# Optimization experiments

Measured on AMD Instinct MI355X. Metric: run time of the kernel, lower is better.

Reference implementation:

```python
import jax, jax.numpy as jnp
import numpy as np

N = 4096
IN_DIM = 256
OUT_DIM = 256
E = 131072


def setup_inputs() -> dict:
    key = jax.random.key(0)
    ks = jax.random.split(key, 8)
    x = jax.random.normal(ks[0], (N, IN_DIM), dtype=jnp.float32)
    edge_index = jax.random.randint(ks[1], (2, E), 0, N, dtype=jnp.int64)
    lap = jax.random.normal(ks[2], (N, N), dtype=jnp.float32)
    d_inv = jax.random.normal(ks[3], (N, N), dtype=jnp.float32)
    # parameters
    W_high = jax.random.normal(ks[4], (IN_DIM, OUT_DIM), dtype=jnp.float32) / np.sqrt(IN_DIM)
    W_conv = jax.random.normal(ks[5], (IN_DIM, OUT_DIM), dtype=jnp.float32) / np.sqrt(IN_DIM)
    b_conv = jnp.zeros((OUT_DIM,), dtype=jnp.float32)
    aL = jax.random.uniform(ks[6], (1,), dtype=jnp.float32)
    aH = jax.random.uniform(ks[7], (1,), dtype=jnp.float32)
    return {"x": x, "edge_index": edge_index, "lap": lap, "d_inv": d_inv,
            "W_high": W_high, "W_conv": W_conv, "b_conv": b_conv,
            "aL": aL, "aH": aH}


def _gcn_conv(x, edge_index, W, b, num_nodes):
    # PyG GCNConv: add self-loops, symmetric normalization, aggregate at target.
    src, dst = edge_index[0], edge_index[1]
    loop = jnp.arange(num_nodes, dtype=edge_index.dtype)
    src_f = jnp.concatenate([src, loop])
    dst_f = jnp.concatenate([dst, loop])
    deg = jax.ops.segment_sum(jnp.ones_like(dst_f, dtype=x.dtype), dst_f,
                              num_segments=num_nodes)
    deg_inv_sqrt = jnp.where(deg > 0, jax.lax.rsqrt(jnp.maximum(deg, 1e-12)), 0.0)
    norm = deg_inv_sqrt[src_f] * deg_inv_sqrt[dst_f]  # [E+N]
    xw = x @ W                                        # [N, out]
    msgs = xw[src_f] * norm[:, None]                  # [E+N, out]
    out = jax.ops.segment_sum(msgs, dst_f, num_segments=num_nodes)
    return out + b


def reference(x, edge_index, lap, d_inv, W_high, W_conv, b_conv, aL, aH):
    # high-pass branch: Lhp = d_inv @ lap @ d_inv; Hh = Lhp @ relu(x @ W_high)
    Lhp = (d_inv @ lap) @ d_inv
    Hh = Lhp @ jax.nn.relu(x @ W_high)
    # low-pass branch: GCNConv
    Hl = _gcn_conv(x, edge_index, W_conv, b_conv, x.shape[0])
    return aL * Hl + aH * Hh
```

## Files before the change

### kernel.cpp

```cpp
#include <hip/hip_runtime.h>

#define NN 4096
#define DD 256
#define EE 131072

typedef __attribute__((ext_vector_type(8))) short s16x8;
typedef __attribute__((ext_vector_type(4))) float f32x4;

__device__ __forceinline__ unsigned short f2bf(float f) {
  unsigned u = __builtin_bit_cast(unsigned, f);
  u += 0x7FFFu + ((u >> 16) & 1u);
  return (unsigned short)(u >> 16);
}

__device__ __forceinline__ ushort4 cvt4(f32x4 v) {
  ushort4 r;
  r.x = f2bf(v[0]); r.y = f2bf(v[1]); r.z = f2bf(v[2]); r.w = f2bf(v[3]);
  return r;
}

__device__ __forceinline__ unsigned cvt2_rhu(float a, float b) {
  unsigned ua = __builtin_bit_cast(unsigned, a) + 0x8000u;
  unsigned ub = __builtin_bit_cast(unsigned, b) + 0x8000u;
  return __builtin_amdgcn_perm(ub, ua, 0x07060302u);
}

__device__ __forceinline__ uint4 pack8(f32x4 a, f32x4 b) {
  uint4 r;
  r.x = cvt2_rhu(a[0], a[1]); r.y = cvt2_rhu(a[2], a[3]);
  r.z = cvt2_rhu(b[0], b[1]); r.w = cvt2_rhu(b[2], b[3]);
  return r;
}


__global__ void k_prep(const int* __restrict__ ei, int* __restrict__ deg,
                       const float* __restrict__ Wh, const float* __restrict__ Wc,
                       unsigned short* __restrict__ WFh, unsigned short* __restrict__ WFc) {
  int t = blockIdx.x * 256 + threadIdx.x;
  if (t < EE) {
    atomicAdd(&deg[ei[EE + t]], 1);
  } else {
    int idx = t - EE;
    int which = idx >> 16;
    int r = idx & 65535;
    int n = r & 255, k = r >> 8;
    const float* W = which ? Wc : Wh;
    unsigned short* WF = which ? WFc : WFh;
    long fidx = ((long)((n >> 4) * 8 + (k >> 5))) * 512 +
                (((k >> 3) & 3) * 16 + (n & 15)) * 8 + (k & 7);
    WF[fidx] = f2bf(W[k * 256 + n]);
  }
}

__global__ void k_scan(const int* __restrict__ deg, int* __restrict__ row_start,
                       float* __restrict__ dis) {
  __shared__ int part[1024];
  int t = threadIdx.x;
  int d0 = deg[4 * t + 0], d1 = deg[4 * t + 1], d2 = deg[4 * t + 2], d3 = deg[4 * t + 3];
  int s = d0 + d1 + d2 + d3;
  part[t] = s;
  __syncthreads();
  for (int off = 1; off < 1024; off <<= 1) {
    int add = (t >= off) ? part[t - off] : 0;
    __syncthreads();
    part[t] += add;
    __syncthreads();
  }
  int base = part[t] - s;
  row_start[4 * t + 0] = base;
  row_start[4 * t + 1] = base + d0;
  row_start[4 * t + 2] = base + d0 + d1;
  row_start[4 * t + 3] = base + d0 + d1 + d2;
  if (t == 1023) row_start[4096] = part[t];
  dis[4 * t + 0] = rsqrtf((float)d0 + 1.0f);
  dis[4 * t + 1] = rsqrtf((float)d1 + 1.0f);
  dis[4 * t + 2] = rsqrtf((float)d2 + 1.0f);
  dis[4 * t + 3] = rsqrtf((float)d3 + 1.0f);
}

__global__ void k_scatter(const int* __restrict__ ei, const int* __restrict__ row_start,
                          int* __restrict__ cursor, int* __restrict__ csr) {
  int e = blockIdx.x * 256 + threadIdx.x;
  if (e < EE) {
    int s = ei[e];
    int d = ei[EE + e];
    int p = atomicAdd(&cursor[d], 1);
    csr[row_start[d] + p] = s;
  }
}

__global__ __launch_bounds__(512) void k_xw(const float* __restrict__ x,
                                            const unsigned short* __restrict__ WFh,
                                            const unsigned short* __restrict__ WFc,
                                            unsigned short* __restrict__ RF,
                                            float* __restrict__ XWs,
                                            const float* __restrict__ dis) {
  __shared__ alignas(16) unsigned short Abuf[16][264];
  const int tid = threadIdx.x;
  const int w = tid >> 6, lane = tid & 63;
  const int quad = lane >> 4, l16 = lane & 15, quad8 = quad * 8;
  const int m0 = blockIdx.x * 16;

  {
    int srow = tid >> 5, scolf = (tid & 31) * 8;
    const float* ap = x + (long)(m0 + srow) * DD + scolf;
    f32x4 a0 = *(const f32x4*)ap;
    f32x4 a1 = *(const f32x4*)(ap + 4);
    *(uint4*)&Abuf[srow][scolf] = pack8(a0, a1);
  }
  __syncthreads();

  const bool hi = (w < 4);
  const int wo = hi ? w : (w - 4);
  const unsigned short* WF = hi ? WFh : WFc;
  const unsigned short* bp = WF + lane * 8;

  f32x4 acc[4] = {{0,0,0,0},{0,0,0,0},{0,0,0,0},{0,0,0,0}};
#pragma unroll
  for (int q = 0; q < 8; ++q) {
    s16x8 af = *(const s16x8*)&Abuf[l16][q * 32 + quad8];
#pragma unroll
    for (int s = 0; s < 4; ++s) {
      s16x8 bf = *(const s16x8*)(bp + ((long)((4 * wo + s) * 8 + q)) * 512);
      acc[s] = __builtin_amdgcn_mfma_f32_16x16x32_bf16(af, bf, acc[s], 0, 0, 0);
    }
  }

  if (hi) {
    const int kc = m0 >> 5;
    const int qp = ((m0 >> 4) & 1) * 2 + (quad >> 1);
    const int j0 = (quad & 1) * 4;
#pragma unroll
    for (int s = 0; s < 4; ++s) {
      int t = 4 * wo + s;
      f32x4 v = acc[s];
      f32x4 z;
      z[0] = v[0] > 0.f ? v[0] : 0.f;
      z[1] = v[1] > 0.f ? v[1] : 0.f;
      z[2] = v[2] > 0.f ? v[2] : 0.f;
      z[3] = v[3] > 0.f ? v[3] : 0.f;
      long idx = ((long)(t * 128 + kc)) * 512 + (qp * 16 + l16) * 8 + j0;
      *(ushort4*)(RF + idx) = cvt4(z);
    }
  } else {
    float dm[4];
#pragma unroll
    for (int r = 0; r < 4; ++r) dm[r] = dis[m0 + quad * 4 + r];
#pragma unroll
    for (int s = 0; s < 4; ++s) {
      int col = 64 * wo + 16 * s + l16;
#pragma unroll
      for (int r = 0; r < 4; ++r)
        XWs[(long)(m0 + quad * 4 + r) * DD + col] = dm[r] * acc[s][r];
    }
  }
}

__global__ void k_agg(const float* __restrict__ XWs, const int* __restrict__ row_start,
                      const int* __restrict__ csr, const float* __restrict__ dis,
                      float* __restrict__ Hl) {
  const int i = blockIdx.x;
  const int t = threadIdx.x;
  const int b0 = row_start[i], b1 = row_start[i + 1];
  float acc = XWs[(long)i * DD + t];
  int j = b0;
  for (; j + 4 <= b1; j += 4) {
    int s0 = csr[j], s1 = csr[j + 1], s2 = csr[j + 2], s3 = csr[j + 3];
    float v0 = XWs[(long)s0 * DD + t];
    float v1 = XWs[(long)s1 * DD + t];
    float v2 = XWs[(long)s2 * DD + t];
    float v3 = XWs[(long)s3 * DD + t];
    acc += (v0 + v1) + (v2 + v3);
  }
  for (; j < b1; ++j) acc += XWs[(long)csr[j] * DD + t];
  Hl[(long)i * DD + t] = dis[i] * acc;
}

template <int EPI>
__global__ __launch_bounds__(512) void k_mm2(const float* __restrict__ A,
                                             const unsigned short* __restrict__ BF,
                                             unsigned short* __restrict__ CF,
                                             float* __restrict__ outF,
                                             const float* __restrict__ Hl,
                                             const float* __restrict__ bconv,
                                             const float* __restrict__ aLp,
                                             const float* __restrict__ aHp) {
  __shared__ alignas(16) unsigned short Abuf[2][32][264];
  const int tid = threadIdx.x;
  const int w = tid >> 6, lane = tid & 63;
  const int quad = lane >> 4, l16 = lane & 15, quad8 = quad * 8;
  const int tile = blockIdx.x & 127, half = blockIdx.x >> 7;
  const int m0 = tile * 32;
  const int tglob = half * 8 + w;

  const int arow = tid >> 4;
  const int acolf = (tid & 15) * 16;
  const float* aptr = A + (long)(m0 + arow) * NN + acolf;

  {
    f32x4 c0 = *(const f32x4*)(aptr + 0);
    f32x4 c1 = *(const f32x4*)(aptr + 4);
    f32x4 c2 = *(const f32x4*)(aptr + 8);
    f32x4 c3 = *(const f32x4*)(aptr + 12);
    *(uint4*)&Abuf[0][arow][acolf] = pack8(c0, c1);
    *(uint4*)&Abuf[0][arow][acolf + 8] = pack8(c2, c3);
  }
  f32x4 anext[4];
#pragma unroll
  for (int i = 0; i < 4; ++i) anext[i] = *(const f32x4*)(aptr + 256 + 4 * i);
  __syncthreads();

  f32x4 acc[2] = {{0,0,0,0},{0,0,0,0}};
  const unsigned short* bbase = BF + ((long)tglob * 128) * 512 + lane * 8;

  for (int s = 0; s < 16; ++s) {
    const int cur = s & 1;
    f32x4 afut[4];
    if (s + 2 < 16) {
#pragma unroll
      for (int i = 0; i < 4; ++i)
        afut[i] = *(const f32x4*)(aptr + (s + 2) * 256 + 4 * i);
    } else {
#pragma unroll
      for (int i = 0; i < 4; ++i) afut[i] = anext[i];
    }

    const unsigned short* bs = bbase + ((long)s * 8) * 512;
#pragma unroll
    for (int c8 = 0; c8 < 8; ++c8) {
      s16x8 bf = *(const s16x8*)(bs + c8 * 512);
      s16x8 a0 = *(const s16x8*)&Abuf[cur][l16][c8 * 32 + quad8];
      s16x8 a1 = *(const s16x8*)&Abuf[cur][16 + l16][c8 * 32 + quad8];
      acc[0] = __builtin_amdgcn_mfma_f32_16x16x32_bf16(a0, bf, acc[0], 0, 0, 0);
      acc[1] = __builtin_amdgcn_mfma_f32_16x16x32_bf16(a1, bf, acc[1], 0, 0, 0);
    }

    if (s + 1 < 16) {
      *(uint4*)&Abuf[1 - cur][arow][acolf] = pack8(anext[0], anext[1]);
      *(uint4*)&Abuf[1 - cur][arow][acolf + 8] = pack8(anext[2], anext[3]);
    }
    __syncthreads();
#pragma unroll
    for (int i = 0; i < 4; ++i) anext[i] = afut[i];
  }

  if constexpr (EPI == 0) {
    const int kc = m0 >> 5;
#pragma unroll
    for (int mu = 0; mu < 2; ++mu) {
      int qp = mu * 2 + (quad >> 1);
      int j0 = (quad & 1) * 4;
      long idx = ((long)(tglob * 128 + kc)) * 512 + (qp * 16 + l16) * 8 + j0;
      *(ushort4*)(CF + idx) = cvt4(acc[mu]);
    }
  } else {
    __shared__ float obuf[32][132];
#pragma unroll
    for (int mu = 0; mu < 2; ++mu)
#pragma unroll
      for (int r = 0; r < 4; ++r)
        obuf[mu * 16 + quad * 4 + r][w * 16 + l16] = acc[mu][r];
    __syncthreads();
    const float aLv = aLp[0], aHv = aHp[0];
    const int orow = tid >> 4;
    const int ocol = (tid & 15) * 8;
    const int gcol = half * 128 + ocol;
#pragma unroll
    for (int j = 0; j < 2; ++j) {
      f32x4 cc = *(const f32x4*)&obuf[orow][ocol + 4 * j];
      f32x4 h = *(const f32x4*)(Hl + (long)(m0 + orow) * DD + gcol + 4 * j);
      f32x4 bc = *(const f32x4*)(bconv + gcol + 4 * j);
      f32x4 res;
      res[0] = aHv * cc[0] + aLv * (h[0] + bc[0]);
      res[1] = aHv * cc[1] + aLv * (h[1] + bc[1]);
      res[2] = aHv * cc[2] + aLv * (h[2] + bc[2]);
      res[3] = aHv * cc[3] + aLv * (h[3] + bc[3]);
      *(f32x4*)(outF + (long)(m0 + orow) * DD + gcol + 4 * j) = res;
    }
  }
}

extern "C" void kernel_launch(void* const* d_in, const int* in_sizes, int n_in,
                              void* d_out, int out_size, void* d_ws, size_t ws_size,
                              hipStream_t stream) {
  const float* x     = (const float*)d_in[0];
  const int*   ei    = (const int*)d_in[1];
  const float* lap   = (const float*)d_in[2];
  const float* dinv  = (const float*)d_in[3];
  const float* Wh    = (const float*)d_in[4];
  const float* Wc    = (const float*)d_in[5];
  const float* bconv = (const float*)d_in[6];
  const float* aL    = (const float*)d_in[7];
  const float* aH    = (const float*)d_in[8];
  float* out = (float*)d_out;
  char* ws = (char*)d_ws;

  int* deg        = (int*)(ws);
  int* cursor     = (int*)(ws + (16 << 10));
  int* row_start  = (int*)(ws + (32 << 10));
  int* csr        = (int*)(ws + (64 << 10));
  float* dis      = (float*)(ws + (576 << 10));
  unsigned short* WFh = (unsigned short*)(ws + (1l << 20));
  unsigned short* WFc = (unsigned short*)(ws + (1l << 20) + (128 << 10));
  unsigned short* RF  = (unsigned short*)(ws + (2l << 20));
  unsigned short* T1F = (unsigned short*)(ws + (4l << 20));
  unsigned short* T2F = (unsigned short*)(ws + (6l << 20));
  float* XWs = (float*)(ws + (8l << 20));
  float* Hl  = (float*)(ws + (12l << 20));

  hipMemsetAsync(ws, 0, 32 << 10, stream);

  k_prep<<<1024, 256, 0, stream>>>(ei, deg, Wh, Wc, WFh, WFc);
  k_scan<<<1, 1024, 0, stream>>>(deg, row_start, dis);
  k_scatter<<<512, 256, 0, stream>>>(ei, row_start, cursor, csr);
  k_xw<<<256, 512, 0, stream>>>(x, WFh, WFc, RF, XWs, dis);
  k_agg<<<4096, 256, 0, stream>>>(XWs, row_start, csr, dis, Hl);

  k_mm2<0><<<256, 512, 0, stream>>>(dinv, RF, T1F, nullptr, nullptr, nullptr, nullptr, nullptr);
  k_mm2<0><<<256, 512, 0, stream>>>(lap, T1F, T2F, nullptr, nullptr, nullptr, nullptr, nullptr);
  k_mm2<3><<<256, 512, 0, stream>>>(dinv, T2F, nullptr, out, Hl, bconv, aL, aH);
}
```

Before: 273.9 us.

## Densify GCN aggregation into normalized adjacency GEMM and split-K all GEMMs

Replaces the CSR build and gather-based aggregation with a dense normalized adjacency matrix M, built by atomic scatter in fragment layout, so the low-pass branch becomes a GEMM. All four 4096x4096x256 products now use a split-K GEMM with 128x256 register tiles, followed by separate reduction kernels. The first dinv GEMM also emits dinv as bf16 fragments so the final GEMM can skip re-converting it. This costs a 64MB memset, a dense GEMM over a mostly-zero matrix, and large partial-sum traffic in exchange for higher MFMA utilization and no irregular gathers.

```diff
diff --git a/kernel.cpp b/kernel.cpp
--- a/kernel.cpp
+++ b/kernel.cpp
@@ -25,11 +25,11 @@
   return __builtin_amdgcn_perm(ub, ua, 0x07060302u);
 }
 
-__device__ __forceinline__ uint4 pack8(f32x4 a, f32x4 b) {
-  uint4 r;
-  r.x = cvt2_rhu(a[0], a[1]); r.y = cvt2_rhu(a[2], a[3]);
-  r.z = cvt2_rhu(b[0], b[1]); r.w = cvt2_rhu(b[2], b[3]);
-  return r;
+__device__ __forceinline__ s16x8 frag_from(f32x4 a, f32x4 b) {
+  uint4 u;
+  u.x = cvt2_rhu(a[0], a[1]); u.y = cvt2_rhu(a[2], a[3]);
+  u.z = cvt2_rhu(b[0], b[1]); u.w = cvt2_rhu(b[2], b[3]);
+  return __builtin_bit_cast(s16x8, u);
 }
 
 
@@ -47,45 +47,31 @@
     const float* W = which ? Wc : Wh;
     unsigned short* WF = which ? WFc : WFh;
     long fidx = ((long)((n >> 4) * 8 + (k >> 5))) * 512 +
-                (((k >> 3) & 3) * 16 + (n & 15)) * 8 + (k & 7);
+                (((k >> 3) & 3) * 128 + (n & 15) * 8 + (k & 7));
     WF[fidx] = f2bf(W[k * 256 + n]);
   }
 }
 
-__global__ void k_scan(const int* __restrict__ deg, int* __restrict__ row_start,
-                       float* __restrict__ dis) {
-  __shared__ int part[1024];
-  int t = threadIdx.x;
-  int d0 = deg[4 * t + 0], d1 = deg[4 * t + 1], d2 = deg[4 * t + 2], d3 = deg[4 * t + 3];
-  int s = d0 + d1 + d2 + d3;
-  part[t] = s;
-  __syncthreads();
-  for (int off = 1; off < 1024; off <<= 1) {
-    int add = (t >= off) ? part[t - off] : 0;
-    __syncthreads();
-    part[t] += add;
-    __syncthreads();
-  }
-  int base = part[t] - s;
-  row_start[4 * t + 0] = base;
-  row_start[4 * t + 1] = base + d0;
-  row_start[4 * t + 2] = base + d0 + d1;
-  row_start[4 * t + 3] = base + d0 + d1 + d2;
-  if (t == 1023) row_start[4096] = part[t];
-  dis[4 * t + 0] = rsqrtf((float)d0 + 1.0f);
-  dis[4 * t + 1] = rsqrtf((float)d1 + 1.0f);
-  dis[4 * t + 2] = rsqrtf((float)d2 + 1.0f);
-  dis[4 * t + 3] = rsqrtf((float)d3 + 1.0f);
-}
-
-__global__ void k_scatter(const int* __restrict__ ei, const int* __restrict__ row_start,
-                          int* __restrict__ cursor, int* __restrict__ csr) {
+__global__ void k_dis(const int* __restrict__ deg, float* __restrict__ dis,
+                      float* __restrict__ M) {
+  int i = blockIdx.x * 256 + threadIdx.x;
+  float d = rsqrtf((float)deg[i] + 1.0f);
+  dis[i] = d;
+  long idx = ((long)((i >> 4) * 128 + (i >> 5))) * 512 +
+             (((i >> 3) & 3) * 128 + (i & 15) * 8 + (i & 7));
+  atomicAdd(&M[idx], d * d);
+}
+
+__global__ void k_scatterM(const int* __restrict__ ei, const float* __restrict__ dis,
+                           float* __restrict__ M) {
   int e = blockIdx.x * 256 + threadIdx.x;
   if (e < EE) {
     int s = ei[e];
     int d = ei[EE + e];
-    int p = atomicAdd(&cursor[d], 1);
-    csr[row_start[d] + p] = s;
+    float v = dis[d] * dis[s];
+    long idx = ((long)((d >> 4) * 128 + (s >> 5))) * 512 +
+               (((s >> 3) & 3) * 128 + (d & 15) * 8 + (s & 7));
+    atomicAdd(&M[idx], v);
   }
 }
 
@@ -93,8 +79,7 @@
                                             const unsigned short* __restrict__ WFh,
                                             const unsigned short* __restrict__ WFc,
                                             unsigned short* __restrict__ RF,
-                                            float* __restrict__ XWs,
-                                            const float* __restrict__ dis) {
+                                            unsigned short* __restrict__ XWcF) {
   __shared__ alignas(16) unsigned short Abuf[16][264];
   const int tid = threadIdx.x;
   const int w = tid >> 6, lane = tid & 63;
@@ -106,13 +91,17 @@
     const float* ap = x + (long)(m0 + srow) * DD + scolf;
     f32x4 a0 = *(const f32x4*)ap;
     f32x4 a1 = *(const f32x4*)(ap + 4);
-    *(uint4*)&Abuf[srow][scolf] = pack8(a0, a1);
+    uint4 u;
+    u.x = cvt2_rhu(a0[0], a0[1]); u.y = cvt2_rhu(a0[2], a0[3]);
+    u.z = cvt2_rhu(a1[0], a1[1]); u.w = cvt2_rhu(a1[2], a1[3]);
+    *(uint4*)&Abuf[srow][scolf] = u;
   }
   __syncthreads();
 
   const bool hi = (w < 4);
   const int wo = hi ? w : (w - 4);
   const unsigned short* WF = hi ? WFh : WFc;
+  unsigned short* OUT = hi ? RF : XWcF;
   const unsigned short* bp = WF + lane * 8;
 
   f32x4 acc[4] = {{0,0,0,0},{0,0,0,0},{0,0,0,0},{0,0,0,0}};
@@ -126,158 +115,181 @@
     }
   }
 
-  if (hi) {
-    const int kc = m0 >> 5;
-    const int qp = ((m0 >> 4) & 1) * 2 + (quad >> 1);
-    const int j0 = (quad & 1) * 4;
-#pragma unroll
-    for (int s = 0; s < 4; ++s) {
-      int t = 4 * wo + s;
-      f32x4 v = acc[s];
-      f32x4 z;
-      z[0] = v[0] > 0.f ? v[0] : 0.f;
-      z[1] = v[1] > 0.f ? v[1] : 0.f;
-      z[2] = v[2] > 0.f ? v[2] : 0.f;
-      z[3] = v[3] > 0.f ? v[3] : 0.f;
-      long idx = ((long)(t * 128 + kc)) * 512 + (qp * 16 + l16) * 8 + j0;
-      *(ushort4*)(RF + idx) = cvt4(z);
-    }
-  } else {
-    float dm[4];
-#pragma unroll
-    for (int r = 0; r < 4; ++r) dm[r] = dis[m0 + quad * 4 + r];
-#pragma unroll
-    for (int s = 0; s < 4; ++s) {
-      int col = 64 * wo + 16 * s + l16;
-#pragma unroll
-      for (int r = 0; r < 4; ++r)
-        XWs[(long)(m0 + quad * 4 + r) * DD + col] = dm[r] * acc[s][r];
-    }
-  }
-}
-
-__global__ void k_agg(const float* __restrict__ XWs, const int* __restrict__ row_start,
-                      const int* __restrict__ csr, const float* __restrict__ dis,
-                      float* __restrict__ Hl) {
-  const int i = blockIdx.x;
-  const int t = threadIdx.x;
-  const int b0 = row_start[i], b1 = row_start[i + 1];
-  float acc = XWs[(long)i * DD + t];
-  int j = b0;
-  for (; j + 4 <= b1; j += 4) {
-    int s0 = csr[j], s1 = csr[j + 1], s2 = csr[j + 2], s3 = csr[j + 3];
-    float v0 = XWs[(long)s0 * DD + t];
-    float v1 = XWs[(long)s1 * DD + t];
-    float v2 = XWs[(long)s2 * DD + t];
-    float v3 = XWs[(long)s3 * DD + t];
-    acc += (v0 + v1) + (v2 + v3);
-  }
-  for (; j < b1; ++j) acc += XWs[(long)csr[j] * DD + t];
-  Hl[(long)i * DD + t] = dis[i] * acc;
-}
-
-template <int EPI>
-__global__ __launch_bounds__(512) void k_mm2(const float* __restrict__ A,
-                                             const unsigned short* __restrict__ BF,
-                                             unsigned short* __restrict__ CF,
-                                             float* __restrict__ outF,
-                                             const float* __restrict__ Hl,
-                                             const float* __restrict__ bconv,
-                                             const float* __restrict__ aLp,
-                                             const float* __restrict__ aHp) {
-  __shared__ alignas(16) unsigned short Abuf[2][32][264];
+  const int kc = m0 >> 5;
+  const int qp = ((m0 >> 4) & 1) * 2 + (quad >> 1);
+  const int j0 = (quad & 1) * 4;
+#pragma unroll
+  for (int s = 0; s < 4; ++s) {
+    int t = 4 * wo + s;
+    f32x4 v = acc[s];
+    if (hi) {
+      v[0] = v[0] > 0.f ? v[0] : 0.f;
+      v[1] = v[1] > 0.f ? v[1] : 0.f;
+      v[2] = v[2] > 0.f ? v[2] : 0.f;
+      v[3] = v[3] > 0.f ? v[3] : 0.f;
+    }
+    long idx = ((long)(t * 128 + kc)) * 512 + (qp * 16 + l16) * 8 + j0;
+    *(ushort4*)(OUT + idx) = cvt4(v);
+  }
+}
+
+template <int AMODE, int EMIT>
+__global__ __launch_bounds__(512) void k_gemm(const float* __restrict__ Afp,
+                                              const unsigned short* __restrict__ AFin,
+                                              const unsigned short* __restrict__ BF,
+                                              float* __restrict__ P,
+                                              unsigned short* __restrict__ AFout) {
   const int tid = threadIdx.x;
   const int w = tid >> 6, lane = tid & 63;
-  const int quad = lane >> 4, l16 = lane & 15, quad8 = quad * 8;
-  const int tile = blockIdx.x & 127, half = blockIdx.x >> 7;
-  const int m0 = tile * 32;
-  const int tglob = half * 8 + w;
-
-  const int arow = tid >> 4;
-  const int acolf = (tid & 15) * 16;
-  const float* aptr = A + (long)(m0 + arow) * NN + acolf;
-
-  {
-    f32x4 c0 = *(const f32x4*)(aptr + 0);
-    f32x4 c1 = *(const f32x4*)(aptr + 4);
-    f32x4 c2 = *(const f32x4*)(aptr + 8);
-    f32x4 c3 = *(const f32x4*)(aptr + 12);
-    *(uint4*)&Abuf[0][arow][acolf] = pack8(c0, c1);
-    *(uint4*)&Abuf[0][arow][acolf + 8] = pack8(c2, c3);
-  }
-  f32x4 anext[4];
-#pragma unroll
-  for (int i = 0; i < 4; ++i) anext[i] = *(const f32x4*)(aptr + 256 + 4 * i);
-  __syncthreads();
-
-  f32x4 acc[2] = {{0,0,0,0},{0,0,0,0}};
-  const unsigned short* bbase = BF + ((long)tglob * 128) * 512 + lane * 8;
-
-  for (int s = 0; s < 16; ++s) {
-    const int cur = s & 1;
-    f32x4 afut[4];
-    if (s + 2 < 16) {
-#pragma unroll
-      for (int i = 0; i < 4; ++i)
-        afut[i] = *(const f32x4*)(aptr + (s + 2) * 256 + 4 * i);
+  const int quad = lane >> 4, l16 = lane & 15;
+  const int mgrp = blockIdx.x & 31, ks = blockIdx.x >> 5;
+  const int m0 = mgrp * 128;
+  const int mh = w & 1, nq = w >> 1;
+  const int kc0 = ks * 16;
+
+  const long mtile0 = (long)(mgrp * 8 + mh * 4);
+  const unsigned short* bptr = BF + (((long)(nq * 4) * 128 + kc0) << 9) + lane * 8;
+  const unsigned short* aptrF = AFin + ((mtile0 * 128 + kc0) << 9) + lane * 8;
+  const float* aptrR = Afp + (long)(m0 + mh * 64 + l16) * NN + kc0 * 32 + quad * 8;
+  const float* aptr2 = Afp + ((mtile0 * 128 + kc0) << 9) + lane * 8;
+  unsigned short* aout = AFout + ((mtile0 * 128 + kc0) << 9) + lane * 8;
+
+  f32x4 acc[4][4];
+#pragma unroll
+  for (int mi = 0; mi < 4; ++mi)
+#pragma unroll
+    for (int ti = 0; ti < 4; ++ti) acc[mi][ti] = (f32x4){0, 0, 0, 0};
+
+  s16x8 bfr[2][4];
+  s16x8 afr[2][4];
+  f32x4 arw[2][8];
+
+#define LOADB(buf, kcv)                                                         \
+  _Pragma("unroll") for (int ti = 0; ti < 4; ++ti)                              \
+      bfr[buf][ti] = *(const s16x8*)(bptr + (((long)(ti * 128 + (kcv))) << 9));
+
+#define LOADA(buf, kcv)                                                         \
+  if (AMODE == 0) {                                                             \
+    _Pragma("unroll") for (int mi = 0; mi < 4; ++mi)                            \
+        afr[buf][mi] = *(const s16x8*)(aptrF + (((long)(mi * 128 + (kcv))) << 9)); \
+  } else if (AMODE == 1) {                                                      \
+    _Pragma("unroll") for (int mi = 0; mi < 4; ++mi) {                          \
+      arw[buf][2 * mi] = *(const f32x4*)(aptrR + (long)mi * 16 * NN + (kcv) * 32); \
+      arw[buf][2 * mi + 1] = *(const f32x4*)(aptrR + (long)mi * 16 * NN + (kcv) * 32 + 4); \
+    }                                                                           \
+  } else {                                                                      \
+    _Pragma("unroll") for (int mi = 0; mi < 4; ++mi) {                          \
+      arw[buf][2 * mi] = *(const f32x4*)(aptr2 + (((long)(mi * 128 + (kcv))) << 9)); \
+      arw[buf][2 * mi + 1] = *(const f32x4*)(aptr2 + (((long)(mi * 128 + (kcv))) << 9) + 4); \
+    }                                                                           \
+  }
+
+  LOADB(0, 0)
+  LOADA(0, 0)
+
+#pragma unroll
+  for (int kc = 0; kc < 16; ++kc) {
+    const int cur = kc & 1, nxt = cur ^ 1;
+    if (kc < 15) {
+      LOADB(nxt, kc + 1)
+      LOADA(nxt, kc + 1)
+    }
+    s16x8 A4[4];
+    if (AMODE == 0) {
+#pragma unroll
+      for (int mi = 0; mi < 4; ++mi) A4[mi] = afr[cur][mi];
     } else {
 #pragma unroll
-      for (int i = 0; i < 4; ++i) afut[i] = anext[i];
-    }
-
-    const unsigned short* bs = bbase + ((long)s * 8) * 512;
-#pragma unroll
-    for (int c8 = 0; c8 < 8; ++c8) {
-      s16x8 bf = *(const s16x8*)(bs + c8 * 512);
-      s16x8 a0 = *(const s16x8*)&Abuf[cur][l16][c8 * 32 + quad8];
-      s16x8 a1 = *(const s16x8*)&Abuf[cur][16 + l16][c8 * 32 + quad8];
-      acc[0] = __builtin_amdgcn_mfma_f32_16x16x32_bf16(a0, bf, acc[0], 0, 0, 0);
-      acc[1] = __builtin_amdgcn_mfma_f32_16x16x32_bf16(a1, bf, acc[1], 0, 0, 0);
-    }
-
-    if (s + 1 < 16) {
-      *(uint4*)&Abuf[1 - cur][arow][acolf] = pack8(anext[0], anext[1]);
-      *(uint4*)&Abuf[1 - cur][arow][acolf + 8] = pack8(anext[2], anext[3]);
-    }
-    __syncthreads();
-#pragma unroll
-    for (int i = 0; i < 4; ++i) anext[i] = afut[i];
-  }
-
-  if constexpr (EPI == 0) {
-    const int kc = m0 >> 5;
-#pragma unroll
-    for (int mu = 0; mu < 2; ++mu) {
-      int qp = mu * 2 + (quad >> 1);
-      int j0 = (quad & 1) * 4;
-      long idx = ((long)(tglob * 128 + kc)) * 512 + (qp * 16 + l16) * 8 + j0;
-      *(ushort4*)(CF + idx) = cvt4(acc[mu]);
-    }
-  } else {
-    __shared__ float obuf[32][132];
-#pragma unroll
-    for (int mu = 0; mu < 2; ++mu)
+      for (int mi = 0; mi < 4; ++mi)
+        A4[mi] = frag_from(arw[cur][2 * mi], arw[cur][2 * mi + 1]);
+    }
+    if (EMIT) {
+      if (nq == 0) {
+#pragma unroll
+        for (int mi = 0; mi < 4; ++mi)
+          *(s16x8*)(aout + (((long)(mi * 128 + kc)) << 9)) = A4[mi];
+      }
+    }
+#pragma unroll
+    for (int ti = 0; ti < 4; ++ti)
+#pragma unroll
+      for (int mi = 0; mi < 4; ++mi)
+        acc[mi][ti] = __builtin_amdgcn_mfma_f32_16x16x32_bf16(A4[mi], bfr[cur][ti], acc[mi][ti], 0, 0, 0);
+  }
+#undef LOADA
+#undef LOADB
+
+  float* pb = P + (long)ks * NN * DD;
+#pragma unroll
+  for (int mi = 0; mi < 4; ++mi) {
+    const int row = m0 + mh * 64 + mi * 16 + quad * 4;
+#pragma unroll
+    for (int ti = 0; ti < 4; ++ti) {
+      const int col = nq * 64 + ti * 16 + l16;
 #pragma unroll
       for (int r = 0; r < 4; ++r)
-        obuf[mu * 16 + quad * 4 + r][w * 16 + l16] = acc[mu][r];
-    __syncthreads();
-    const float aLv = aLp[0], aHv = aHp[0];
-    const int orow = tid >> 4;
-    const int ocol = (tid & 15) * 8;
-    const int gcol = half * 128 + ocol;
-#pragma unroll
-    for (int j = 0; j < 2; ++j) {
-      f32x4 cc = *(const f32x4*)&obuf[orow][ocol + 4 * j];
-      f32x4 h = *(const f32x4*)(Hl + (long)(m0 + orow) * DD + gcol + 4 * j);
-      f32x4 bc = *(const f32x4*)(bconv + gcol + 4 * j);
-      f32x4 res;
-      res[0] = aHv * cc[0] + aLv * (h[0] + bc[0]);
-      res[1] = aHv * cc[1] + aLv * (h[1] + bc[1]);
-      res[2] = aHv * cc[2] + aLv * (h[2] + bc[2]);
-      res[3] = aHv * cc[3] + aLv * (h[3] + bc[3]);
-      *(f32x4*)(outF + (long)(m0 + orow) * DD + gcol + 4 * j) = res;
-    }
-  }
+        pb[(long)(row + r) * DD + col] = acc[mi][ti][r];
+    }
+  }
+}
+
+__global__ void k_redF(const float* __restrict__ P, unsigned short* __restrict__ TF) {
+  const int tid = threadIdx.x;
+  const int w = tid >> 6, lane = tid & 63;
+  const int quad = lane >> 4, l16 = lane & 15;
+#pragma unroll
+  for (int c = 0; c < 2; ++c) {
+    int cid = blockIdx.x * 8 + w * 2 + c;
+    int ntile = cid >> 7, kchunk = cid & 127;
+    int n = ntile * 16 + l16;
+    int kbase = kchunk * 32 + quad * 8;
+    float v[8];
+#pragma unroll
+    for (int j = 0; j < 8; ++j) v[j] = 0.f;
+#pragma unroll
+    for (int s = 0; s < 8; ++s) {
+      const float* p = P + (long)s * NN * DD;
+#pragma unroll
+      for (int j = 0; j < 8; ++j) v[j] += p[(long)(kbase + j) * DD + n];
+    }
+    ushort4 o0, o1;
+    o0.x = f2bf(v[0]); o0.y = f2bf(v[1]); o0.z = f2bf(v[2]); o0.w = f2bf(v[3]);
+    o1.x = f2bf(v[4]); o1.y = f2bf(v[5]); o1.z = f2bf(v[6]); o1.w = f2bf(v[7]);
+    *(ushort4*)(TF + (long)cid * 512 + lane * 8) = o0;
+    *(ushort4*)(TF + (long)cid * 512 + lane * 8 + 4) = o1;
+  }
+}
+
+__global__ void k_redHl(const float* __restrict__ P, float* __restrict__ Hl) {
+  long off = ((long)blockIdx.x * 256 + threadIdx.x) * 4;
+  f32x4 v = {0, 0, 0, 0};
+#pragma unroll
+  for (int s = 0; s < 8; ++s) {
+    f32x4 p = *(const f32x4*)(P + (long)s * NN * DD + off);
+    v[0] += p[0]; v[1] += p[1]; v[2] += p[2]; v[3] += p[3];
+  }
+  *(f32x4*)(Hl + off) = v;
+}
+
+__global__ void k_final(const float* __restrict__ P, const float* __restrict__ Hl,
+                        const float* __restrict__ bconv, const float* __restrict__ aLp,
+                        const float* __restrict__ aHp, float* __restrict__ out) {
+  long off = ((long)blockIdx.x * 256 + threadIdx.x) * 4;
+  f32x4 v = {0, 0, 0, 0};
+#pragma unroll
+  for (int s = 0; s < 8; ++s) {
+    f32x4 p = *(const f32x4*)(P + (long)s * NN * DD + off);
+    v[0] += p[0]; v[1] += p[1]; v[2] += p[2]; v[3] += p[3];
+  }
+  const float aLv = aLp[0], aHv = aHp[0];
+  f32x4 h = *(const f32x4*)(Hl + off);
+  f32x4 b = *(const f32x4*)(bconv + (int)(off & 255));
+  f32x4 res;
+  res[0] = aHv * v[0] + aLv * (h[0] + b[0]);
+  res[1] = aHv * v[1] + aLv * (h[1] + b[1]);
+  res[2] = aHv * v[2] + aLv * (h[2] + b[2]);
+  res[3] = aHv * v[3] + aLv * (h[3] + b[3]);
+  *(f32x4*)(out + off) = res;
 }
 
 extern "C" void kernel_launch(void* const* d_in, const int* in_sizes, int n_in,
@@ -294,29 +306,39 @@
   const float* aH    = (const float*)d_in[8];
   float* out = (float*)d_out;
   char* ws = (char*)d_ws;
-
-  int* deg        = (int*)(ws);
-  int* cursor     = (int*)(ws + (16 << 10));
-  int* row_start  = (int*)(ws + (32 << 10));
-  int* csr        = (int*)(ws + (64 << 10));
-  float* dis      = (float*)(ws + (576 << 10));
-  unsigned short* WFh = (unsigned short*)(ws + (1l << 20));
-  unsigned short* WFc = (unsigned short*)(ws + (1l << 20) + (128 << 10));
-  unsigned short* RF  = (unsigned short*)(ws + (2l << 20));
-  unsigned short* T1F = (unsigned short*)(ws + (4l << 20));
-  unsigned short* T2F = (unsigned short*)(ws + (6l << 20));
-  float* XWs = (float*)(ws + (8l << 20));
-  float* Hl  = (float*)(ws + (12l << 20));
-
-  hipMemsetAsync(ws, 0, 32 << 10, stream);
+  const long MB = 1l << 20;
+
+  float* M              = (float*)(ws);
+  unsigned short* dinvF = (unsigned short*)(ws);
+  float* P              = (float*)(ws + 64 * MB);
+  unsigned short* WFh   = (unsigned short*)(ws + 96 * MB);
+  unsigned short* WFc   = (unsigned short*)(ws + 96 * MB + 128 * 1024);
+  unsigned short* RF    = (unsigned short*)(ws + 97 * MB);
+  unsigned short* XWcF  = (unsigned short*)(ws + 99 * MB);
+  unsigned short* T1F   = (unsigned short*)(ws + 101 * MB);
+  unsigned short* T2F   = (unsigned short*)(ws + 103 * MB);
+  float* Hl             = (float*)(ws + 105 * MB);
+  int* deg              = (int*)(ws + 109 * MB);
+  float* dis            = (float*)(ws + 109 * MB + 16 * 1024);
+
+  hipMemsetAsync(M, 0, 64 * MB, stream);
+  hipMemsetAsync(deg, 0, 16 * 1024, stream);
 
   k_prep<<<1024, 256, 0, stream>>>(ei, deg, Wh, Wc, WFh, WFc);
-  k_scan<<<1, 1024, 0, stream>>>(deg, row_start, dis);
-  k_scatter<<<512, 256, 0, stream>>>(ei, row_start, cursor, csr);
-  k_xw<<<256, 512, 0, stream>>>(x, WFh, WFc, RF, XWs, dis);
-  k_agg<<<4096, 256, 0, stream>>>(XWs, row_start, csr, dis, Hl);
-
-  k_mm2<0><<<256, 512, 0, stream>>>(dinv, RF, T1F, nullptr, nullptr, nullptr, nullptr, nullptr);
-  k_mm2<0><<<256, 512, 0, stream>>>(lap, T1F, T2F, nullptr, nullptr, nullptr, nullptr, nullptr);
-  k_mm2<3><<<256, 512, 0, stream>>>(dinv, T2F, nullptr, out, Hl, bconv, aL, aH);
-}
+  k_dis<<<16, 256, 0, stream>>>(deg, dis, M);
+  k_scatterM<<<512, 256, 0, stream>>>(ei, dis, M);
+  k_xw<<<256, 512, 0, stream>>>(x, WFh, WFc, RF, XWcF);
+
+  k_gemm<2, 0><<<256, 512, 0, stream>>>(M, nullptr, XWcF, P, nullptr);
+  k_redHl<<<1024, 256, 0, stream>>>(P, Hl);
+
+  k_gemm<1, 1><<<256, 512, 0, stream>>>(dinv, nullptr, RF, P, dinvF);
+  k_redF<<<256, 256, 0, stream>>>(P, T1F);
+
+  k_gemm<1, 0><<<256, 512, 0, stream>>>(lap, nullptr, T1F, P, nullptr);
+  k_redF<<<256, 256, 0, stream>>>(P, T2F);
+
+  k_gemm<0, 0><<<256, 512, 0, stream>>>(nullptr, dinvF, T2F, P, nullptr);
+
+  k_final<<<1024, 256, 0, stream>>>(P, Hl, bconv, aL, aH, out);
+}
```

Measured after the change: 360.8 us. 1.32x slower.
